# Optimization experiments

Hardware: AMD Instinct MI355X
Metric: run time of the kernel (lower is better)

Reference implementation:

```python
import jax, jax.numpy as jnp
import numpy as np

B, S, D, HID, H, VOCAB, DFF = 4, 2048, 512, 512, 8, 32000, 2048
DK = HID // H   # per-head Q/K dim
DV = D // H     # per-head V dim


def sinusoidal_pe(L, d):
    pos = jnp.arange(L, dtype=jnp.float32)[:, None]
    i = jnp.arange(d, dtype=jnp.float32)[None, :]
    ang = pos / jnp.power(jnp.float32(10000.0), i / d)
    return jnp.where(jnp.arange(d)[None, :] % 2 == 0, jnp.sin(ang), jnp.cos(ang))  # [L, d]


def layer_norm(x, gamma, beta, eps=1e-5):
    mu = jnp.mean(x, axis=-1, keepdims=True)
    var = jnp.mean((x - mu) ** 2, axis=-1, keepdims=True)
    return (x - mu) * jax.lax.rsqrt(var + eps) * gamma + beta


def setup_inputs() -> dict:
    key = jax.random.key(0)
    ks = jax.random.split(key, 24)
    n = lambda k, shape, fan: jax.random.normal(k, shape, dtype=jnp.float32) / np.sqrt(fan)
    inp = {
        'x': jax.random.randint(ks[0], (B, S), 0, VOCAB),
        'emb': n(ks[1], (VOCAB, D), D),
        'WfQ': n(ks[2], (D, HID), D), 'bfQ': jnp.zeros((HID,), jnp.float32),
        'WfK': n(ks[3], (D, HID), D), 'bfK': jnp.zeros((HID,), jnp.float32),
        'WfV': n(ks[4], (D, D), D),   'bfV': jnp.zeros((D,), jnp.float32),
        'WQ': n(ks[5], (H, HID, DK), HID), 'bQ': jnp.zeros((H, DK), jnp.float32),
        'WK': n(ks[6], (H, HID, DK), HID), 'bK': jnp.zeros((H, DK), jnp.float32),
        'WV': n(ks[7], (H, D, DV), D),     'bV': jnp.zeros((H, DV), jnp.float32),
        'Wo': n(ks[8], (D, D), D),   'bo': jnp.zeros((D,), jnp.float32),
        'W1': n(ks[9], (D, DFF), D), 'b1': jnp.zeros((DFF,), jnp.float32),
        'W2': n(ks[10], (DFF, D), DFF), 'b2': jnp.zeros((D,), jnp.float32),
        'gamma': jnp.ones((D,), jnp.float32), 'beta': jnp.zeros((D,), jnp.float32),
    }
    return inp


def reference(x, emb, WfQ, bfQ, WfK, bfK, WfV, bfV, WQ, bQ, WK, bK, WV, bV,
              Wo, bo, W1, b1, W2, b2, gamma, beta):
    z = emb[x] + sinusoidal_pe(x.shape[1], D)[None]            # [B,S,D]
    Q = z @ WfQ + bfQ                                           # [B,S,HID]
    K = z @ WfK + bfK
    V = z @ WfV + bfV                                           # [B,S,D]
    # per-head projections (batched equivalent of the per-head Linear loop)
    Qh = jnp.einsum('bsd,hdk->bhsk', Q, WQ) + bQ[None, :, None, :]  # [B,H,S,DK]
    Kh = jnp.einsum('bsd,hdk->bhsk', K, WK) + bK[None, :, None, :]
    Vh = jnp.einsum('bsd,hdv->bhsv', V, WV) + bV[None, :, None, :]  # [B,H,S,DV]
    scores = jnp.einsum('bhqk,bhsk->bhqs', Qh, Kh) / np.sqrt(DK)    # [B,H,S,S]
    attn = jax.nn.softmax(scores, axis=-1)
    heads = jnp.einsum('bhqs,bhsv->bhqv', attn, Vh)                 # [B,H,S,DV]
    concat = heads.transpose(0, 2, 1, 3).reshape(x.shape[0], x.shape[1], D)
    attn_out = concat @ Wo + bo
    a = layer_norm(attn_out + z, gamma, beta)
    ffn = jax.nn.relu(a @ W1 + b1) @ W2 + b2
    out = layer_norm(ffn + a, gamma, beta)   # same (shared) LayerNorm params, as in source
    return jax.nn.relu(out)
```

## Files before the change

kernel.cpp:

```cpp
#include <hip/hip_runtime.h>
#include <math.h>

typedef __bf16 bf16;
typedef __bf16 bf16x8 __attribute__((ext_vector_type(8)));
typedef __bf16 bf16x4 __attribute__((ext_vector_type(4)));
typedef _Float16 f16;
typedef _Float16 f16x8 __attribute__((ext_vector_type(8)));
typedef _Float16 f16x4 __attribute__((ext_vector_type(4)));
typedef _Float16 f16x2 __attribute__((ext_vector_type(2)));
typedef __fp16 h16x2 __attribute__((ext_vector_type(2)));
typedef float f32x4 __attribute__((ext_vector_type(4)));
typedef unsigned int u32;

#define S_LEN 2048
#define QSCALE 0.18033688011112042f

#if __has_builtin(__builtin_amdgcn_exp2f)
#define EXP2(x) __builtin_amdgcn_exp2f(x)
#else
#define EXP2(x) exp2f(x)
#endif

__device__ __forceinline__ void gload_lds16(const void* g, void* l) {
  __builtin_amdgcn_global_load_lds((const __attribute__((address_space(1))) u32*)g,
                                   (__attribute__((address_space(3))) u32*)l, 16, 0, 0);
}

__global__ __launch_bounds__(256) void embed_pe(const int* __restrict__ x,
    const float* __restrict__ emb, bf16* __restrict__ zb)
{
  const int row = blockIdx.x;
  const int s = row & (S_LEN - 1);
  const int tok = x[row];
  const float* e = emb + (size_t)tok * 512;
  bf16* zbr = zb + (size_t)row * 512;
  for (int i = threadIdx.x; i < 512; i += 256) {
    float invf = __expf((float)i * (-9.210340371976184f / 512.0f));
    float ang = (float)s * invf;
    float pe = (i & 1) ? __cosf(ang) : __sinf(ang);
    zbr[i] = (bf16)(e[i] + pe);
  }
}

__global__ __launch_bounds__(256) void conv_t(
    const float* __restrict__ Wo, const float* __restrict__ W1, const float* __restrict__ W2,
    const float* __restrict__ WQ, const float* __restrict__ WK, const float* __restrict__ WV,
    const float* __restrict__ WfQ, const float* __restrict__ WfK, const float* __restrict__ WfV,
    const float* __restrict__ bfQ, const float* __restrict__ bfK, const float* __restrict__ bfV,
    const float* __restrict__ bQ, const float* __restrict__ bK, const float* __restrict__ bV,
    bf16* __restrict__ wot, bf16* __restrict__ w1t, bf16* __restrict__ w2t,
    bf16* __restrict__ wqt, bf16* __restrict__ wkt, bf16* __restrict__ wvt,
    bf16* __restrict__ wfqp, bf16* __restrict__ wfkp, bf16* __restrict__ wfvp,
    float* __restrict__ bc)
{
  __shared__ float T[64][65];
  const int y = blockIdx.y, x = blockIdx.x;
  if (y == 9) {
    int n = x * 4 + ((int)threadIdx.x >> 6);
    int lane = threadIdx.x & 63;
    int z = n >> 9, hk = n & 511, h = hk >> 6, k = hk & 63;
    const float* bf = z == 0 ? bfQ : (z == 1 ? bfK : bfV);
    const float* W  = z == 0 ? WQ  : (z == 1 ? WK  : WV);
    const float* bH = z == 0 ? bQ  : (z == 1 ? bK  : bV);
    float s = 0.f;
    for (int e = lane; e < 512; e += 64)
      s += bf[e] * W[((size_t)h * 512 + e) * 64 + k];
    #pragma unroll
    for (int m = 1; m < 64; m <<= 1) s += __shfl_xor(s, m, 64);
    if (lane == 0) {
      float v = s + bH[h * 64 + k];
      if (z == 0) v *= QSCALE;
      bc[n] = v;
    }
    return;
  }
  if (y >= 6) {
    if (x >= 256) return;
    int g = x * 256 + threadIdx.x;
    const float* in = y == 6 ? WfQ : (y == 7 ? WfK : WfV);
    bf16* outp = y == 6 ? wfqp : (y == 7 ? wfkp : wfvp);
    float4 v = *(const float4*)(in + (size_t)g * 4);
    bf16x4 o = {(bf16)v.x, (bf16)v.y, (bf16)v.z, (bf16)v.w};
    *(bf16x4*)(outp + (size_t)g * 4) = o;
    return;
  }
  const int tx = threadIdx.x & 63, ty = threadIdx.x >> 6;
  const float* src; bf16* dst;
  int src_cols, dst_cols; float scale = 1.f;
  if (y == 0) {
    if (x >= 64) return;
    int kt = x & 7, nt = x >> 3;
    src = Wo + (size_t)(kt * 64) * 512 + nt * 64; src_cols = 512;
    dst = wot + (size_t)(nt * 64) * 512 + kt * 64; dst_cols = 512;
  } else if (y == 1) {
    if (x >= 256) return;
    int kt = x & 7, nt = x >> 3;
    src = W1 + (size_t)(kt * 64) * 2048 + nt * 64; src_cols = 2048;
    dst = w1t + (size_t)(nt * 64) * 512 + kt * 64; dst_cols = 512;
  } else if (y == 2) {
    if (x >= 256) return;
    int kt = x & 31, nt = x >> 5;
    src = W2 + (size_t)(kt * 64) * 512 + nt * 64; src_cols = 512;
    dst = w2t + (size_t)(nt * 64) * 2048 + kt * 64; dst_cols = 2048;
  } else {
    if (x >= 64) return;
    const float* W = y == 3 ? WQ : (y == 4 ? WK : WV);
    bf16* o = y == 3 ? wqt : (y == 4 ? wkt : wvt);
    if (y == 3) scale = QSCALE;
    int h = x >> 3, rt = x & 7;
    src = W + (size_t)(h * 512 + rt * 64) * 64; src_cols = 64;
    dst = o + (size_t)(h * 64) * 512 + rt * 64; dst_cols = 512;
  }
  #pragma unroll
  for (int i = 0; i < 16; i++) {
    int rr = i * 4 + ty;
    T[rr][tx] = src[(size_t)rr * src_cols + tx];
  }
  __syncthreads();
  #pragma unroll
  for (int i = 0; i < 16; i++) {
    int rr = i * 4 + ty;
    dst[(size_t)rr * dst_cols + tx] = (bf16)(T[tx][rr] * scale);
  }
}

__global__ __launch_bounds__(256) void gemm_comb(
    const bf16* __restrict__ wqt, const bf16* __restrict__ wkt, const bf16* __restrict__ wvt,
    const bf16* __restrict__ wfqp, const bf16* __restrict__ wfkp, const bf16* __restrict__ wfvp,
    bf16* __restrict__ wc)
{
  __shared__ bf16 As[128 * 32];
  __shared__ bf16 Bs[64 * 32];
  const int z = blockIdx.z;
  const bf16* A  = z == 0 ? wqt : (z == 1 ? wkt : wvt);
  const bf16* Bt = z == 0 ? wfqp : (z == 1 ? wfkp : wfvp);
  bf16* outb = wc + (size_t)z * 262144;
  const int tid = threadIdx.x;
  const int wave = tid >> 6, lane = tid & 63, quad = lane >> 4, l16 = lane & 15;
  const int row0 = blockIdx.x * 128, col0 = blockIdx.y * 64;
  const int wm = wave >> 1, wn = wave & 1;
  f32x4 acc[4][2] = {};

  for (int kk = 0; kk < 512; kk += 32) {
    __syncthreads();
    #pragma unroll
    for (int r = 0; r < 2; r++) {
      int c = r * 256 + tid;
      gload_lds16(A + (size_t)(row0 + (c >> 2)) * 512 + kk + (c & 3) * 8, As + c * 8);
    }
    gload_lds16(Bt + (size_t)(col0 + (tid >> 2)) * 512 + kk + (tid & 3) * 8, Bs + tid * 8);
    __syncthreads();
    bf16x8 af[4], bfr[2];
    #pragma unroll
    for (int i = 0; i < 4; i++)
      af[i] = *(const bf16x8*)(As + (wm * 64 + i * 16 + l16) * 32 + quad * 8);
    #pragma unroll
    for (int i = 0; i < 2; i++)
      bfr[i] = *(const bf16x8*)(Bs + (wn * 32 + i * 16 + l16) * 32 + quad * 8);
    #pragma unroll
    for (int mt = 0; mt < 4; mt++)
      #pragma unroll
      for (int nt = 0; nt < 2; nt++)
        acc[mt][nt] = __builtin_amdgcn_mfma_f32_16x16x32_bf16(af[mt], bfr[nt], acc[mt][nt], 0, 0, 0);
  }
  #pragma unroll
  for (int nt = 0; nt < 2; nt++) {
    int col = col0 + wn * 32 + nt * 16 + l16;
    #pragma unroll
    for (int mt = 0; mt < 4; mt++) {
      int rowb = row0 + wm * 64 + mt * 16 + quad * 4;
      #pragma unroll
      for (int i = 0; i < 4; i++)
        outb[(size_t)(rowb + i) * 512 + col] = (bf16)acc[mt][nt][i];
    }
  }
}

#define GEMM_CORE(A_, Bt_, K_, KK0_, ITERS_)                                            \
  bf16x8 ar0, ar1, br0, br1;                                                            \
  const int c0 = tid, c1 = 256 + tid;                                                   \
  const size_t aoff0 = (size_t)(row0 + (c0 >> 2)) * (K_) + (c0 & 3) * 8;                \
  const size_t aoff1 = (size_t)(row0 + (c1 >> 2)) * (K_) + (c1 & 3) * 8;                \
  const size_t boff0 = (size_t)(col0 + (c0 >> 2)) * (K_) + (c0 & 3) * 8;                \
  const size_t boff1 = (size_t)(col0 + (c1 >> 2)) * (K_) + (c1 & 3) * 8;                \
  ar0 = *(const bf16x8*)((A_) + aoff0 + (KK0_));                                        \
  ar1 = *(const bf16x8*)((A_) + aoff1 + (KK0_));                                        \
  br0 = *(const bf16x8*)((Bt_) + boff0 + (KK0_));                                       \
  br1 = *(const bf16x8*)((Bt_) + boff1 + (KK0_));                                       \
  for (int it = 0; it < (ITERS_); it++) {                                               \
    bf16* AsB = As[it & 1];                                                             \
    bf16* BsB = Bs[it & 1];                                                             \
    *(bf16x8*)(AsB + c0 * 8) = ar0;                                                     \
    *(bf16x8*)(AsB + c1 * 8) = ar1;                                                     \
    *(bf16x8*)(BsB + c0 * 8) = br0;                                                     \
    *(bf16x8*)(BsB + c1 * 8) = br1;                                                     \
    __syncthreads();                                                                    \
    if (it + 1 < (ITERS_)) {                                                            \
      int kk = (KK0_) + (it + 1) * 32;                                                  \
      ar0 = *(const bf16x8*)((A_) + aoff0 + kk);                                        \
      ar1 = *(const bf16x8*)((A_) + aoff1 + kk);                                        \
      br0 = *(const bf16x8*)((Bt_) + boff0 + kk);                                      \
      br1 = *(const bf16x8*)((Bt_) + boff1 + kk);                                      \
    }                                                                                   \
    bf16x8 af[4], bfr[4];                                                               \
    _Pragma("unroll")                                                                   \
    for (int i = 0; i < 4; i++)                                                         \
      af[i] = *(const bf16x8*)(AsB + (wm * 64 + i * 16 + l16) * 32 + quad * 8);         \
    _Pragma("unroll")                                                                   \
    for (int i = 0; i < 4; i++)                                                         \
      bfr[i] = *(const bf16x8*)(BsB + (wn * 64 + i * 16 + l16) * 32 + quad * 8);        \
    _Pragma("unroll")                                                                   \
    for (int mt = 0; mt < 4; mt++)                                                      \
      _Pragma("unroll")                                                                 \
      for (int nt = 0; nt < 4; nt++)                                                    \
        acc[mt][nt] = __builtin_amdgcn_mfma_f32_16x16x32_bf16(af[mt], bfr[nt], acc[mt][nt], 0, 0, 0); \
  }

__global__ __launch_bounds__(256) void gemm_bt(
    const bf16* __restrict__ A, const bf16* __restrict__ Bt,
    const float* __restrict__ bias, bf16* __restrict__ outb,
    int M, int N, int K, int relu)
{
  __shared__ bf16 As[2][4096];
  __shared__ bf16 Bs[2][4096];
  const int tid = threadIdx.x;
  const int wave = tid >> 6, lane = tid & 63, quad = lane >> 4, l16 = lane & 15;
  const int row0 = blockIdx.x * 128, col0 = blockIdx.y * 128;
  const int wm = wave >> 1, wn = wave & 1;
  f32x4 acc[4][4] = {};
  GEMM_CORE(A, Bt, K, 0, K / 32)

  #pragma unroll
  for (int nt = 0; nt < 4; nt++) {
    int col = col0 + wn * 64 + nt * 16 + l16;
    float bv = bias[col];
    #pragma unroll
    for (int mt = 0; mt < 4; mt++) {
      int rowb = row0 + wm * 64 + mt * 16 + quad * 4;
      #pragma unroll
      for (int i = 0; i < 4; i++) {
        float v = acc[mt][nt][i] + bv;
        if (relu) v = fmaxf(v, 0.f);
        outb[(size_t)(rowb + i) * N + col] = (bf16)v;
      }
    }
  }
}

__global__ __launch_bounds__(256) void gemm_qkv(
    const bf16* __restrict__ A, const bf16* __restrict__ Bt,
    const float* __restrict__ bias, f16* __restrict__ qk, f16* __restrict__ Vt)
{
  __shared__ bf16 As[2][4096];
  __shared__ bf16 Bs[2][4096];
  const int tid = threadIdx.x;
  const int wave = tid >> 6, lane = tid & 63, quad = lane >> 4, l16 = lane & 15;
  const int row0 = blockIdx.x * 128, col0 = blockIdx.y * 128;
  const int wm = wave >> 1, wn = wave & 1;
  f32x4 acc[4][4] = {};
  GEMM_CORE(A, Bt, 512, 0, 16)

  #pragma unroll
  for (int nt = 0; nt < 4; nt++) {
    int col = col0 + wn * 64 + nt * 16 + l16;
    float bv = bias[col];
    if (col < 1024) {
      #pragma unroll
      for (int mt = 0; mt < 4; mt++) {
        int rowb = row0 + wm * 64 + mt * 16 + quad * 4;
        #pragma unroll
        for (int i = 0; i < 4; i++)
          qk[(size_t)(rowb + i) * 1024 + col] = (f16)(acc[mt][nt][i] + bv);
      }
    } else {
      int h = (col - 1024) >> 6, dv = col & 63;
      #pragma unroll
      for (int mt = 0; mt < 4; mt++) {
        int rowb = row0 + wm * 64 + mt * 16 + quad * 4;
        int b = rowb >> 11, s = rowb & 2047;
        f16x4 vv;
        #pragma unroll
        for (int i = 0; i < 4; i++) vv[i] = (f16)(acc[mt][nt][i] + bv);
        *(f16x4*)(Vt + ((size_t)((b * 8 + h) * 64 + dv)) * 2048 + s) = vv;
      }
    }
  }
}

__global__ __launch_bounds__(256) void gemm_part(
    const bf16* __restrict__ A, const bf16* __restrict__ Bt,
    bf16* __restrict__ Pa, bf16* __restrict__ Pb, int N, int K, int Kh)
{
  __shared__ bf16 As[2][4096];
  __shared__ bf16 Bs[2][4096];
  const int tid = threadIdx.x;
  const int wave = tid >> 6, lane = tid & 63, quad = lane >> 4, l16 = lane & 15;
  const int row0 = blockIdx.x * 128, col0 = blockIdx.y * 128;
  const int wm = wave >> 1, wn = wave & 1;
  const int kk0 = blockIdx.z * Kh;
  bf16* P = blockIdx.z ? Pb : Pa;
  f32x4 acc[4][4] = {};
  GEMM_CORE(A, Bt, K, kk0, Kh / 32)

  #pragma unroll
  for (int nt = 0; nt < 4; nt++) {
    int col = col0 + wn * 64 + nt * 16 + l16;
    #pragma unroll
    for (int mt = 0; mt < 4; mt++) {
      int rowb = row0 + wm * 64 + mt * 16 + quad * 4;
      #pragma unroll
      for (int i = 0; i < 4; i++)
        P[(size_t)(rowb + i) * N + col] = (bf16)acc[mt][nt][i];
    }
  }
}

__global__ __launch_bounds__(256) void gemm_wo(
    const bf16* __restrict__ Op, const float* __restrict__ Rp,
    const bf16* __restrict__ Bt, bf16* __restrict__ Pa, bf16* __restrict__ Pb)
{
  __shared__ bf16 As[2][4096];
  __shared__ bf16 Bs[2][4096];
  const int tid = threadIdx.x;
  const int wave = tid >> 6, lane = tid & 63, quad = lane >> 4, l16 = lane & 15;
  const int row0 = blockIdx.x * 128, col0 = blockIdx.y * 128;
  const int wm = wave >> 1, wn = wave & 1;
  const int kk0 = blockIdx.z * 256;
  bf16* P = blockIdx.z ? Pb : Pa;
  f32x4 acc[4][4] = {};

  const int c0 = tid, c1 = 256 + tid;
  const int r0 = row0 + (c0 >> 2), r1 = r0 + 64;
  const int b0 = r0 >> 11, s0 = r0 & 2047;
  const int b1 = r1 >> 11, s1 = r1 & 2047;
  const int ccol = (c0 & 3) * 8;
  const int h0 = kk0 >> 6;
  const size_t boff0 = (size_t)(col0 + (c0 >> 2)) * 512 + ccol;
  const size_t boff1 = (size_t)(col0 + 64 + (c0 >> 2)) * 512 + ccol;

  float inv0[4], inv1[4];
  #pragma unroll
  for (int hh = 0; hh < 4; hh++) {
    int hg = h0 + hh;
    int ra = (b0 * 8 + hg) * 2048 + s0;
    float r = (Rp[ra] + Rp[65536 + ra]) + (Rp[131072 + ra] + Rp[196608 + ra]);
    inv0[hh] = 1.f / r;
    int rb = (b1 * 8 + hg) * 2048 + s1;
    r = (Rp[rb] + Rp[65536 + rb]) + (Rp[131072 + rb] + Rp[196608 + rb]);
    inv1[hh] = 1.f / r;
  }

  bf16x8 p0q[4], p1q[4], br0, br1;
  {
    int hg = h0, dv = ccol;
    size_t ia0 = ((size_t)(b0 * 8 + hg) * 2048 + s0) * 64 + dv;
    size_t ia1 = ((size_t)(b1 * 8 + hg) * 2048 + s1) * 64 + dv;
    #pragma unroll
    for (int q = 0; q < 4; q++) {
      p0q[q] = *(const bf16x8*)(Op + q * 4194304ull + ia0);
      p1q[q] = *(const bf16x8*)(Op + q * 4194304ull + ia1);
    }
    br0 = *(const bf16x8*)(Bt + boff0 + kk0);
    br1 = *(const bf16x8*)(Bt + boff1 + kk0);
  }

  for (int it = 0; it < 8; it++) {
    bf16* AsB = As[it & 1];
    bf16* BsB = Bs[it & 1];
    const float iv0 = inv0[it >> 1], iv1 = inv1[it >> 1];
    bf16x8 a0v, a1v;
    #pragma unroll
    for (int i = 0; i < 8; i++) {
      float v0 = ((float)p0q[0][i] + (float)p0q[1][i]) + ((float)p0q[2][i] + (float)p0q[3][i]);
      float v1 = ((float)p1q[0][i] + (float)p1q[1][i]) + ((float)p1q[2][i] + (float)p1q[3][i]);
      a0v[i] = (bf16)(v0 * iv0);
      a1v[i] = (bf16)(v1 * iv1);
    }
    *(bf16x8*)(AsB + c0 * 8) = a0v;
    *(bf16x8*)(AsB + c1 * 8) = a1v;
    *(bf16x8*)(BsB + c0 * 8) = br0;
    *(bf16x8*)(BsB + c1 * 8) = br1;
    __syncthreads();
    if (it < 7) {
      int itn = it + 1;
      int kk = kk0 + itn * 32;
      int hg = h0 + (itn >> 1);
      int dv = (itn & 1) * 32 + ccol;
      size_t ia0 = ((size_t)(b0 * 8 + hg) * 2048 + s0) * 64 + dv;
      size_t ia1 = ((size_t)(b1 * 8 + hg) * 2048 + s1) * 64 + dv;
      #pragma unroll
      for (int q = 0; q < 4; q++) {
        p0q[q] = *(const bf16x8*)(Op + q * 4194304ull + ia0);
        p1q[q] = *(const bf16x8*)(Op + q * 4194304ull + ia1);
      }
      br0 = *(const bf16x8*)(Bt + boff0 + kk);
      br1 = *(const bf16x8*)(Bt + boff1 + kk);
    }
    bf16x8 af[4], bfr[4];
    #pragma unroll
    for (int i = 0; i < 4; i++)
      af[i] = *(const bf16x8*)(AsB + (wm * 64 + i * 16 + l16) * 32 + quad * 8);
    #pragma unroll
    for (int i = 0; i < 4; i++)
      bfr[i] = *(const bf16x8*)(BsB + (wn * 64 + i * 16 + l16) * 32 + quad * 8);
    #pragma unroll
    for (int mt = 0; mt < 4; mt++)
      #pragma unroll
      for (int nt = 0; nt < 4; nt++)
        acc[mt][nt] = __builtin_amdgcn_mfma_f32_16x16x32_bf16(af[mt], bfr[nt], acc[mt][nt], 0, 0, 0);
  }

  #pragma unroll
  for (int nt = 0; nt < 4; nt++) {
    int col = col0 + wn * 64 + nt * 16 + l16;
    #pragma unroll
    for (int mt = 0; mt < 4; mt++) {
      int rowb = row0 + wm * 64 + mt * 16 + quad * 4;
      #pragma unroll
      for (int i = 0; i < 4; i++)
        P[(size_t)(rowb + i) * 512 + col] = (bf16)acc[mt][nt][i];
    }
  }
}

__global__ __launch_bounds__(256, 2) void flash_attn(
    const f16* __restrict__ qk, const f16* __restrict__ Vt,
    bf16* __restrict__ Op, float* __restrict__ Rp)
{
  __shared__ f16 Ks[2][4096];
  __shared__ f16 Vs[2][4096];
  const int bh = blockIdx.y, b = bh >> 3, h = bh & 7;
  const int q0 = blockIdx.x * 128;
  const int quarter = blockIdx.z;
  const int tid = threadIdx.x;
  const int wave = tid >> 6, lane = tid & 63, quad = lane >> 4, l16 = lane & 15;

  const f16* Qb = qk + ((size_t)b * S_LEN) * 1024 + h * 64;
  const f16* Kb = Qb + 512;
  const f16* Vtb = Vt + ((size_t)bh * 64) * 2048;
  const int key0 = quarter * 512;

  f16x8 qf[2][2];
  #pragma unroll
  for (int f = 0; f < 2; f++) {
    int qrow = q0 + wave * 32 + f * 16 + l16;
    #pragma unroll
    for (int kh = 0; kh < 2; kh++)
      qf[f][kh] = *(const f16x8*)(Qb + (size_t)qrow * 1024 + kh * 32 + quad * 8);
  }

  f32x4 O[2][4] = {};
  f32x4 Osum[2] = {};
  const f16x4 onesA = {(f16)1.f, (f16)1.f, (f16)1.f, (f16)1.f};
  const int swz = l16 & 7;

  f16x8 kreg[2], vreg[2];
  const int srow = tid >> 3, soff = tid & 7;
  const int srow1 = srow + 32;

  {
    int kb = key0;
    kreg[0] = *(const f16x8*)(Kb + (size_t)(kb + srow) * 1024 + soff * 8);
    vreg[0] = *(const f16x8*)(Vtb + (size_t)srow * 2048 + kb + soff * 8);
    kreg[1] = *(const f16x8*)(Kb + (size_t)(kb + srow1) * 1024 + soff * 8);
    vreg[1] = *(const f16x8*)(Vtb + (size_t)srow1 * 2048 + kb + soff * 8);
  }

  for (int c = 0; c < 8; c++) {
    f16* KsB = Ks[c & 1];
    f16* VsB = Vs[c & 1];
    *(f16x8*)(KsB + srow * 64 + ((soff ^ (srow & 7)) * 8)) = kreg[0];
    *(f16x8*)(VsB + srow * 64 + ((soff ^ (srow & 7)) * 8)) = vreg[0];
    *(f16x8*)(KsB + srow1 * 64 + ((soff ^ (srow1 & 7)) * 8)) = kreg[1];
    *(f16x8*)(VsB + srow1 * 64 + ((soff ^ (srow1 & 7)) * 8)) = vreg[1];
    __syncthreads();
    if (c < 7) {
      int kb = key0 + (c + 1) * 64;
      kreg[0] = *(const f16x8*)(Kb + (size_t)(kb + srow) * 1024 + soff * 8);
      vreg[0] = *(const f16x8*)(Vtb + (size_t)srow * 2048 + kb + soff * 8);
      kreg[1] = *(const f16x8*)(Kb + (size_t)(kb + srow1) * 1024 + soff * 8);
      vreg[1] = *(const f16x8*)(Vtb + (size_t)srow1 * 2048 + kb + soff * 8);
    }

    #pragma unroll
    for (int nt = 0; nt < 4; nt++) {
      const f16* kp = KsB + (nt * 16 + l16) * 64;
      f16x8 kf0 = *(const f16x8*)(kp + ((quad ^ swz) * 8));
      f16x8 kf1 = *(const f16x8*)(kp + (((4 + quad) ^ swz) * 8));
      f16x4 pf[2];
      f32x4 a0 = {}, a1 = {};
      __builtin_amdgcn_s_setprio(1);
      a0 = __builtin_amdgcn_mfma_f32_16x16x32_f16(kf0, qf[0][0], a0, 0, 0, 0);
      a0 = __builtin_amdgcn_mfma_f32_16x16x32_f16(kf1, qf[0][1], a0, 0, 0, 0);
      a1 = __builtin_amdgcn_mfma_f32_16x16x32_f16(kf0, qf[1][0], a1, 0, 0, 0);
      a1 = __builtin_amdgcn_mfma_f32_16x16x32_f16(kf1, qf[1][1], a1, 0, 0, 0);
      __builtin_amdgcn_s_setprio(0);
      #pragma unroll
      for (int f = 0; f < 2; f++) {
        const f32x4& a = f == 0 ? a0 : a1;
        float e0 = EXP2(a[0]);
        float e1 = EXP2(a[1]);
        float e2 = EXP2(a[2]);
        float e3 = EXP2(a[3]);
        h16x2 lo = __builtin_amdgcn_cvt_pkrtz(e0, e1);
        h16x2 hi = __builtin_amdgcn_cvt_pkrtz(e2, e3);
        f16x2 lo2 = __builtin_bit_cast(f16x2, lo);
        f16x2 hi2 = __builtin_bit_cast(f16x2, hi);
        pf[f] = __builtin_shufflevector(lo2, hi2, 0, 1, 2, 3);
        Osum[f] = __builtin_amdgcn_mfma_f32_16x16x16f16(onesA, pf[f], Osum[f], 0, 0, 0);
      }
      int vchunk = nt * 2 + (quad >> 1);
      __builtin_amdgcn_s_setprio(1);
      #pragma unroll
      for (int mt = 0; mt < 4; mt++) {
        const f16* vp = VsB + (mt * 16 + l16) * 64 + ((vchunk ^ swz) * 8) + (quad & 1) * 4;
        f16x4 vf = *(const f16x4*)vp;
        #pragma unroll
        for (int f = 0; f < 2; f++)
          O[f][mt] = __builtin_amdgcn_mfma_f32_16x16x16f16(vf, pf[f], O[f][mt], 0, 0, 0);
      }
      __builtin_amdgcn_s_setprio(0);
    }
  }

  #pragma unroll
  for (int f = 0; f < 2; f++) {
    bf16* ob = (f == 0 ? (bf16*)&Ks[0][0] : (bf16*)&Vs[0][0]) + wave * 1024;
    #pragma unroll
    for (int mt = 0; mt < 4; mt++) {
      bf16x4 w;
      #pragma unroll
      for (int i = 0; i < 4; i++) w[i] = (bf16)O[f][mt][i];
      int chunk = mt * 2 + (quad >> 1);
      *(bf16x4*)(ob + l16 * 64 + ((chunk ^ (l16 & 7)) << 3) + (quad & 1) * 4) = w;
    }
  }
  asm volatile("s_waitcnt lgkmcnt(0)" ::: "memory");
  const size_t obase = (size_t)(quarter * 32 + bh) * 2048;
  #pragma unroll
  for (int f = 0; f < 2; f++) {
    const bf16* ob = (f == 0 ? (const bf16*)&Ks[0][0] : (const bf16*)&Vs[0][0]) + wave * 1024;
    int row = lane >> 2, cc = (lane & 3) * 2;
    bf16x8 o0 = *(const bf16x8*)(ob + row * 64 + ((cc ^ (row & 7)) << 3));
    bf16x8 o1 = *(const bf16x8*)(ob + row * 64 + (((cc + 1) ^ (row & 7)) << 3));
    size_t g = (obase + q0 + wave * 32 + f * 16 + row) * 64 + (lane & 3) * 16;
    *(bf16x8*)(Op + g) = o0;
    *(bf16x8*)(Op + g + 8) = o1;
    if (quad == f)
      Rp[obase + q0 + wave * 32 + f * 16 + l16] = Osum[f][0];
  }
}

__global__ __launch_bounds__(256) void ln_merge(const bf16* __restrict__ Pa,
    const bf16* __restrict__ Pb, const float* __restrict__ badd,
    const bf16* __restrict__ resid, const float* __restrict__ gamma,
    const float* __restrict__ beta, float* __restrict__ outf,
    bf16* __restrict__ outb, int relu)
{
  const int row = blockIdx.x * 4 + (threadIdx.x >> 6);
  const int lane = threadIdx.x & 63;
  const size_t base = (size_t)row * 512;
  const int e0 = lane * 8;
  bf16x8 pa = *(const bf16x8*)(Pa + base + e0);
  bf16x8 pb = *(const bf16x8*)(Pb + base + e0);
  bf16x8 rr = *(const bf16x8*)(resid + base + e0);
  float4 C0 = *(const float4*)(badd + e0);
  float4 C1 = *(const float4*)(badd + e0 + 4);
  float v[8];
  v[0] = (float)pa[0] + (float)pb[0] + (float)rr[0] + C0.x;
  v[1] = (float)pa[1] + (float)pb[1] + (float)rr[1] + C0.y;
  v[2] = (float)pa[2] + (float)pb[2] + (float)rr[2] + C0.z;
  v[3] = (float)pa[3] + (float)pb[3] + (float)rr[3] + C0.w;
  v[4] = (float)pa[4] + (float)pb[4] + (float)rr[4] + C1.x;
  v[5] = (float)pa[5] + (float)pb[5] + (float)rr[5] + C1.y;
  v[6] = (float)pa[6] + (float)pb[6] + (float)rr[6] + C1.z;
  v[7] = (float)pa[7] + (float)pb[7] + (float)rr[7] + C1.w;
  float s = 0.f;
  #pragma unroll
  for (int i = 0; i < 8; i++) s += v[i];
  #pragma unroll
  for (int m = 1; m < 64; m <<= 1) s += __shfl_xor(s, m, 64);
  float mu = s * (1.f / 512.f);
  float d[8], q = 0.f;
  #pragma unroll
  for (int i = 0; i < 8; i++) { d[i] = v[i] - mu; q += d[i] * d[i]; }
  #pragma unroll
  for (int m = 1; m < 64; m <<= 1) q += __shfl_xor(q, m, 64);
  float rsn = rsqrtf(q * (1.f / 512.f) + 1e-5f);
  float4 g0 = *(const float4*)(gamma + e0);
  float4 g1 = *(const float4*)(gamma + e0 + 4);
  float4 b0 = *(const float4*)(beta + e0);
  float4 b1 = *(const float4*)(beta + e0 + 4);
  float y[8];
  y[0] = d[0] * rsn * g0.x + b0.x; y[1] = d[1] * rsn * g0.y + b0.y;
  y[2] = d[2] * rsn * g0.z + b0.z; y[3] = d[3] * rsn * g0.w + b0.w;
  y[4] = d[4] * rsn * g1.x + b1.x; y[5] = d[5] * rsn * g1.y + b1.y;
  y[6] = d[6] * rsn * g1.z + b1.z; y[7] = d[7] * rsn * g1.w + b1.w;
  if (relu) {
    #pragma unroll
    for (int i = 0; i < 8; i++) y[i] = fmaxf(y[i], 0.f);
  }
  if (outf) {
    float4 o0 = {y[0], y[1], y[2], y[3]}, o1 = {y[4], y[5], y[6], y[7]};
    *(float4*)(outf + base + e0) = o0;
    *(float4*)(outf + base + e0 + 4) = o1;
  }
  if (outb) {
    bf16x8 ob;
    #pragma unroll
    for (int i = 0; i < 8; i++) ob[i] = (bf16)y[i];
    *(bf16x8*)(outb + base + e0) = ob;
  }
}

extern "C" void kernel_launch(void* const* d_in, const int* in_sizes, int n_in,
                              void* d_out, int out_size, void* d_ws, size_t ws_size,
                              hipStream_t stream)
{
  const int*   x    = (const int*)  d_in[0];
  const float* emb  = (const float*)d_in[1];
  const float* WfQ  = (const float*)d_in[2];
  const float* bfQv = (const float*)d_in[3];
  const float* WfK  = (const float*)d_in[4];
  const float* bfKv = (const float*)d_in[5];
  const float* WfV  = (const float*)d_in[6];
  const float* bfVv = (const float*)d_in[7];
  const float* WQ   = (const float*)d_in[8];
  const float* bQ   = (const float*)d_in[9];
  const float* WK   = (const float*)d_in[10];
  const float* bK   = (const float*)d_in[11];
  const float* WV   = (const float*)d_in[12];
  const float* bV   = (const float*)d_in[13];
  const float* Wo   = (const float*)d_in[14];
  const float* bo   = (const float*)d_in[15];
  const float* W1   = (const float*)d_in[16];
  const float* b1   = (const float*)d_in[17];
  const float* W2   = (const float*)d_in[18];
  const float* b2   = (const float*)d_in[19];
  const float* gamma= (const float*)d_in[20];
  const float* beta = (const float*)d_in[21];
  float* out = (float*)d_out;

  char* ws = (char*)d_ws;
  const size_t MB = 1024ull * 1024;
  bf16*  bz   = (bf16*) (ws);
  f16*   qkh  = (f16*)  (ws + 8 * MB);
  f16*   Vt   = (f16*)  (ws + 24 * MB);
  bf16*  Op   = (bf16*) (ws + 32 * MB);
  float* Rp   = (float*)(ws + 64 * MB);
  bf16*  PaW  = (bf16*) (ws + 8 * MB);
  bf16*  PbW  = (bf16*) (ws + 16 * MB);
  bf16*  ffn1 = (bf16*) (ws + 8 * MB);
  bf16*  Pa2  = (bf16*) (ws + 40 * MB);
  bf16*  Pb2  = (bf16*) (ws + 48 * MB);
  char* wp = ws + 74 * MB;
  bf16* wfqp = (bf16*)(wp);
  bf16* wfkp = (bf16*)(wp + 512 * 1024);
  bf16* wfvp = (bf16*)(wp + 1024 * 1024);
  bf16* wqt  = (bf16*)(wp + 1536 * 1024);
  bf16* wkt  = (bf16*)(wp + 2048 * 1024);
  bf16* wvt  = (bf16*)(wp + 2560 * 1024);
  bf16* wc   = (bf16*)(wp + 3072 * 1024);
  bf16* wot  = (bf16*)(wp + 4608 * 1024);
  bf16* w1t  = (bf16*)(wp + 5120 * 1024);
  bf16* w2t  = (bf16*)(wp + 7168 * 1024);
  float* bc  = (float*)(wp + 9216 * 1024);

  conv_t<<<dim3(384, 10), 256, 0, stream>>>(Wo, W1, W2, WQ, WK, WV, WfQ, WfK, WfV,
                                            bfQv, bfKv, bfVv, bQ, bK, bV,
                                            wot, w1t, w2t, wqt, wkt, wvt,
                                            wfqp, wfkp, wfvp, bc);
  gemm_comb<<<dim3(4, 8, 3), 256, 0, stream>>>(wqt, wkt, wvt, wfqp, wfkp, wfvp, wc);

  embed_pe<<<8192, 256, 0, stream>>>(x, emb, bz);

  gemm_qkv<<<dim3(64, 12), 256, 0, stream>>>(bz, wc, bc, qkh, Vt);
  flash_attn<<<dim3(16, 32, 4), 256, 0, stream>>>(qkh, Vt, Op, Rp);

  gemm_wo<<<dim3(64, 4, 2), 256, 0, stream>>>(Op, Rp, wot, PaW, PbW);
  ln_merge<<<2048, 256, 0, stream>>>(PaW, PbW, bo, bz, gamma, beta, nullptr, bz, 0);
  gemm_bt<<<dim3(64, 16), 256, 0, stream>>>(bz, w1t, b1, ffn1, 8192, 2048, 512, 1);
  gemm_part<<<dim3(64, 4, 2), 256, 0, stream>>>(ffn1, w2t, Pa2, Pb2, 512, 2048, 1024);
  ln_merge<<<2048, 256, 0, stream>>>(Pa2, Pb2, b2, bz, gamma, beta, out, nullptr, 1);
}
```

Before: 315.0 us.

## Stage V transpose through LDS, split W2 GEMM four ways, split attention launch

The V-column blocks of the QKV GEMM now write their tile transposed into shared memory first. They then emit contiguous f16x4 rows into Vt, replacing strided scattered stores. The second FFN GEMM uses a 4-way split-K with two extra partial buffers, and ln_merge sums them, to give more blocks for parallelism. This costs extra partial-buffer traffic. Flash attention is also issued as two launches over halves of the batch-head range, which adds a launch.

```diff
diff --git a/kernel.cpp b/kernel.cpp
--- a/kernel.cpp
+++ b/kernel.cpp
@@ -251,8 +251,9 @@
     const bf16* __restrict__ A, const bf16* __restrict__ Bt,
     const float* __restrict__ bias, f16* __restrict__ qk, f16* __restrict__ Vt)
 {
-  __shared__ bf16 As[2][4096];
-  __shared__ bf16 Bs[2][4096];
+  __shared__ char ldsbuf[32768];
+  bf16 (*As)[4096] = (bf16(*)[4096])ldsbuf;
+  bf16 (*Bs)[4096] = (bf16(*)[4096])(ldsbuf + 16384);
   const int tid = threadIdx.x;
   const int wave = tid >> 6, lane = tid & 63, quad = lane >> 4, l16 = lane & 15;
   const int row0 = blockIdx.x * 128, col0 = blockIdx.y * 128;
@@ -260,36 +261,54 @@
   f32x4 acc[4][4] = {};
   GEMM_CORE(A, Bt, 512, 0, 16)
 
+  if (col0 >= 1024) {
+    f16* Vst = (f16*)ldsbuf;
+    const int h0 = (col0 - 1024) >> 6;
+    const int b = row0 >> 11, s0 = row0 & 2047;
+    __syncthreads();
+    #pragma unroll
+    for (int nt = 0; nt < 4; nt++) {
+      int c = wn * 64 + nt * 16 + l16;
+      float bv = bias[col0 + c];
+      #pragma unroll
+      for (int mt = 0; mt < 4; mt++) {
+        int chunk = wm * 16 + mt * 4 + quad;
+        f16x4 vv;
+        #pragma unroll
+        for (int i = 0; i < 4; i++) vv[i] = (f16)(acc[mt][nt][i] + bv);
+        *(f16x4*)(Vst + c * 128 + ((chunk ^ ((c & 7) << 2)) * 4)) = vv;
+      }
+    }
+    __syncthreads();
+    #pragma unroll
+    for (int p = 0; p < 16; p++) {
+      int c = p * 8 + (tid >> 5);
+      int ch = tid & 31;
+      f16x4 vv = *(const f16x4*)(Vst + c * 128 + ((ch ^ ((c & 7) << 2)) * 4));
+      int h = h0 + (c >> 6), dv = c & 63;
+      *(f16x4*)(Vt + ((size_t)((b * 8 + h) * 64 + dv)) * 2048 + s0 + ch * 4) = vv;
+    }
+    return;
+  }
+
   #pragma unroll
   for (int nt = 0; nt < 4; nt++) {
     int col = col0 + wn * 64 + nt * 16 + l16;
     float bv = bias[col];
-    if (col < 1024) {
-      #pragma unroll
-      for (int mt = 0; mt < 4; mt++) {
-        int rowb = row0 + wm * 64 + mt * 16 + quad * 4;
-        #pragma unroll
-        for (int i = 0; i < 4; i++)
-          qk[(size_t)(rowb + i) * 1024 + col] = (f16)(acc[mt][nt][i] + bv);
-      }
-    } else {
-      int h = (col - 1024) >> 6, dv = col & 63;
-      #pragma unroll
-      for (int mt = 0; mt < 4; mt++) {
-        int rowb = row0 + wm * 64 + mt * 16 + quad * 4;
-        int b = rowb >> 11, s = rowb & 2047;
-        f16x4 vv;
-        #pragma unroll
-        for (int i = 0; i < 4; i++) vv[i] = (f16)(acc[mt][nt][i] + bv);
-        *(f16x4*)(Vt + ((size_t)((b * 8 + h) * 64 + dv)) * 2048 + s) = vv;
-      }
+    #pragma unroll
+    for (int mt = 0; mt < 4; mt++) {
+      int rowb = row0 + wm * 64 + mt * 16 + quad * 4;
+      #pragma unroll
+      for (int i = 0; i < 4; i++)
+        qk[(size_t)(rowb + i) * 1024 + col] = (f16)(acc[mt][nt][i] + bv);
     }
   }
 }
 
 __global__ __launch_bounds__(256) void gemm_part(
     const bf16* __restrict__ A, const bf16* __restrict__ Bt,
-    bf16* __restrict__ Pa, bf16* __restrict__ Pb, int N, int K, int Kh)
+    bf16* __restrict__ Pa, bf16* __restrict__ Pb,
+    bf16* __restrict__ Pc, bf16* __restrict__ Pd, int N, int K, int Kh)
 {
   __shared__ bf16 As[2][4096];
   __shared__ bf16 Bs[2][4096];
@@ -298,7 +317,7 @@
   const int row0 = blockIdx.x * 128, col0 = blockIdx.y * 128;
   const int wm = wave >> 1, wn = wave & 1;
   const int kk0 = blockIdx.z * Kh;
-  bf16* P = blockIdx.z ? Pb : Pa;
+  bf16* P = blockIdx.z == 0 ? Pa : (blockIdx.z == 1 ? Pb : (blockIdx.z == 2 ? Pc : Pd));
   f32x4 acc[4][4] = {};
   GEMM_CORE(A, Bt, K, kk0, Kh / 32)
 
@@ -425,11 +444,11 @@
 
 __global__ __launch_bounds__(256, 2) void flash_attn(
     const f16* __restrict__ qk, const f16* __restrict__ Vt,
-    bf16* __restrict__ Op, float* __restrict__ Rp)
+    bf16* __restrict__ Op, float* __restrict__ Rp, int bh0)
 {
   __shared__ f16 Ks[2][4096];
   __shared__ f16 Vs[2][4096];
-  const int bh = blockIdx.y, b = bh >> 3, h = bh & 7;
+  const int bh = blockIdx.y + bh0, b = bh >> 3, h = bh & 7;
   const int q0 = blockIdx.x * 128;
   const int quarter = blockIdx.z;
   const int tid = threadIdx.x;
@@ -552,10 +571,10 @@
 }
 
 __global__ __launch_bounds__(256) void ln_merge(const bf16* __restrict__ Pa,
-    const bf16* __restrict__ Pb, const float* __restrict__ badd,
-    const bf16* __restrict__ resid, const float* __restrict__ gamma,
-    const float* __restrict__ beta, float* __restrict__ outf,
-    bf16* __restrict__ outb, int relu)
+    const bf16* __restrict__ Pb, const bf16* __restrict__ Pc, const bf16* __restrict__ Pd,
+    const float* __restrict__ badd, const bf16* __restrict__ resid,
+    const float* __restrict__ gamma, const float* __restrict__ beta,
+    float* __restrict__ outf, bf16* __restrict__ outb, int relu)
 {
   const int row = blockIdx.x * 4 + (threadIdx.x >> 6);
   const int lane = threadIdx.x & 63;
@@ -575,6 +594,12 @@
   v[5] = (float)pa[5] + (float)pb[5] + (float)rr[5] + C1.y;
   v[6] = (float)pa[6] + (float)pb[6] + (float)rr[6] + C1.z;
   v[7] = (float)pa[7] + (float)pb[7] + (float)rr[7] + C1.w;
+  if (Pc) {
+    bf16x8 pc = *(const bf16x8*)(Pc + base + e0);
+    bf16x8 pd = *(const bf16x8*)(Pd + base + e0);
+    #pragma unroll
+    for (int i = 0; i < 8; i++) v[i] += (float)pc[i] + (float)pd[i];
+  }
   float s = 0.f;
   #pragma unroll
   for (int i = 0; i < 8; i++) s += v[i];
@@ -653,6 +678,8 @@
   bf16*  ffn1 = (bf16*) (ws + 8 * MB);
   bf16*  Pa2  = (bf16*) (ws + 40 * MB);
   bf16*  Pb2  = (bf16*) (ws + 48 * MB);
+  bf16*  Pc2  = (bf16*) (ws + 56 * MB);
+  bf16*  Pd2  = (bf16*) (ws + 64 * MB);
   char* wp = ws + 74 * MB;
   bf16* wfqp = (bf16*)(wp);
   bf16* wfkp = (bf16*)(wp + 512 * 1024);
@@ -675,11 +702,13 @@
   embed_pe<<<8192, 256, 0, stream>>>(x, emb, bz);
 
   gemm_qkv<<<dim3(64, 12), 256, 0, stream>>>(bz, wc, bc, qkh, Vt);
-  flash_attn<<<dim3(16, 32, 4), 256, 0, stream>>>(qkh, Vt, Op, Rp);
+  flash_attn<<<dim3(16, 16, 4), 256, 0, stream>>>(qkh, Vt, Op, Rp, 0);
+  flash_attn<<<dim3(16, 16, 4), 256, 0, stream>>>(qkh, Vt, Op, Rp, 16);
 
   gemm_wo<<<dim3(64, 4, 2), 256, 0, stream>>>(Op, Rp, wot, PaW, PbW);
-  ln_merge<<<2048, 256, 0, stream>>>(PaW, PbW, bo, bz, gamma, beta, nullptr, bz, 0);
+  ln_merge<<<2048, 256, 0, stream>>>(PaW, PbW, nullptr, nullptr, bo, bz, gamma, beta,
+                                     nullptr, bz, 0);
   gemm_bt<<<dim3(64, 16), 256, 0, stream>>>(bz, w1t, b1, ffn1, 8192, 2048, 512, 1);
-  gemm_part<<<dim3(64, 4, 2), 256, 0, stream>>>(ffn1, w2t, Pa2, Pb2, 512, 2048, 1024);
-  ln_merge<<<2048, 256, 0, stream>>>(Pa2, Pb2, b2, bz, gamma, beta, out, nullptr, 1);
-}
+  gemm_part<<<dim3(64, 4, 4), 256, 0, stream>>>(ffn1, w2t, Pa2, Pb2, Pc2, Pd2, 512, 2048, 512);
+  ln_merge<<<2048, 256, 0, stream>>>(Pa2, Pb2, Pc2, Pd2, b2, bz, gamma, beta, out, nullptr, 1);
+}
```

Result: slower. 333.0 us (+5.7%).
